# Kernel optimization log

Hardware: AMD Instinct MI355X
Metric: run time of the kernel (lower is better)

Reference implementation:

```python
import jax, jax.numpy as jnp
import numpy as np

B, S, H = 32, 2048, 1024


def setup_inputs() -> dict:
    key = jax.random.key(0)
    k1, k2, k3, k4, k5, k6 = jax.random.split(key, 6)
    hidden = jax.random.normal(k1, (B, H), dtype=jnp.float32)
    encoder_outputs = jax.random.normal(k2, (B, S, H), dtype=jnp.float32)
    lengths = jax.random.randint(k3, (B,), 1, S + 1, dtype=jnp.int64)
    scale = 1.0 / np.sqrt(H)
    Wq = jax.random.normal(k4, (H, H), dtype=jnp.float32) * scale
    Wk = jax.random.normal(k5, (H, H), dtype=jnp.float32) * scale
    v = jax.random.uniform(k6, (H,), dtype=jnp.float32)  # torch.rand init
    return {"hidden": hidden, "encoder_outputs": encoder_outputs,
            "lengths": lengths, "Wq": Wq, "Wk": Wk, "v": v}


def reference(hidden, encoder_outputs, lengths, Wq, Wk, v):
    # query: (B, 1, H); nn.Linear(bias=False) applies x @ W.T
    query = (hidden @ Wq.T)[:, None, :]
    keys = jnp.einsum('bsh,kh->bsk', encoder_outputs, Wk)  # (B, S, H)
    energy = jnp.tanh(query + keys)                         # (B, S, H)
    attn = jnp.einsum('bsh,h->bs', energy, v)               # (B, S)
    seq = encoder_outputs.shape[1]
    mask = jnp.arange(seq)[None, :] < lengths[:, None]      # (B, S)
    attn = jnp.where(mask, attn, -jnp.inf)
    return jax.nn.softmax(attn, axis=1)
```

## Files before the change

kernel.cpp:

```cpp
#include <hip/hip_runtime.h>
#include <hip/hip_fp16.h>
#include <stdint.h>

#define B_SZ 32
#define S_SZ 2048
#define H_SZ 1024
#define M_SZ (B_SZ * S_SZ)

typedef _Float16 half8 __attribute__((ext_vector_type(8)));
typedef float floatx4 __attribute__((ext_vector_type(4)));

struct h4 { _Float16 x, y, z, w; };

__global__ __launch_bounds__(256) void convert_f32_to_f16(
    const float* __restrict__ in, h4* __restrict__ out, int n4) {
  int i = blockIdx.x * blockDim.x + threadIdx.x;
  int stride = gridDim.x * blockDim.x;
  const float4* in4 = (const float4*)in;
  for (; i < n4; i += stride) {
    float4 f = in4[i];
    h4 o;
    o.x = (_Float16)f.x; o.y = (_Float16)f.y;
    o.z = (_Float16)f.z; o.w = (_Float16)f.w;
    out[i] = o;
  }
}

__global__ __launch_bounds__(256) void query_kernel(
    const float* __restrict__ hidden, const float* __restrict__ Wq,
    float* __restrict__ q) {
  int t = blockIdx.x * blockDim.x + threadIdx.x;
  int b = t & 31;
  int n = t >> 5;
  const float4* h4p = (const float4*)(hidden + (size_t)b * H_SZ);
  const float4* w4p = (const float4*)(Wq + (size_t)n * H_SZ);
  float acc = 0.f;
  #pragma unroll 4
  for (int i = 0; i < H_SZ / 4; ++i) {
    float4 h = h4p[i], w = w4p[i];
    acc = fmaf(h.x, w.x, acc);
    acc = fmaf(h.y, w.y, acc);
    acc = fmaf(h.z, w.z, acc);
    acc = fmaf(h.w, w.w, acc);
  }
  q[(size_t)b * H_SZ + n] = acc;
}

__device__ __forceinline__ void gl_lds16(const void* g, void* l) {
  __builtin_amdgcn_global_load_lds(
      (const __attribute__((address_space(1))) void*)g,
      (__attribute__((address_space(3))) void*)l,
      16, 0, 0);
}

__device__ __forceinline__ float fast_tanh(float x) {
  float ax = fabsf(x);
  float e = __expf(ax * -2.0f);
  float t = (1.0f - e) / (1.0f + e);
  return copysignf(t, x);
}

#define TILE 128
#define BK 32

__global__ __launch_bounds__(256) void fused_keys_kernel(
    const float* __restrict__ A,
    const _Float16* __restrict__ Bt,
    const float* __restrict__ q,
    const float* __restrict__ v,
    float* __restrict__ partial)
{
  __shared__ __align__(16) float    As[TILE * BK];
  __shared__ __align__(16) _Float16 Bs[TILE * BK];
  __shared__ float rowsum[TILE];
  __shared__ float q_l[TILE];
  __shared__ float v_l[TILE];

  const int tid  = threadIdx.x;
  const int w    = tid >> 6;
  const int lane = tid & 63;

  const int hw   = blockIdx.x;
  const int xcd  = hw & 7;
  const int slot = hw >> 3;
  const int bn   = slot & 7;
  const int bm   = ((slot >> 3) << 3) | xcd;

  const int R0   = bm * TILE;
  const int C0   = bn * TILE;
  const int bidx = R0 >> 11;

  if (tid < TILE) {
    q_l[tid] = q[(size_t)bidx * H_SZ + C0 + tid];
    v_l[tid] = v[C0 + tid];
    rowsum[tid] = 0.f;
  }

  const int wm = w >> 1, wn = w & 1;
  const int cL = lane & 15, quad = lane >> 4;

  floatx4 acc[4][4];
  #pragma unroll
  for (int m = 0; m < 4; ++m)
    #pragma unroll
    for (int n = 0; n < 4; ++n)
      acc[m][n] = (floatx4){0.f, 0.f, 0.f, 0.f};

  const int arow_l = lane >> 3;
  const int ap     = lane & 7;
  const int brow_l = lane >> 2;
  const int bp     = lane & 3;

  const float*    Ablk = A  + (size_t)R0 * H_SZ;
  const _Float16* Bblk = Bt + (size_t)C0 * H_SZ;

  for (int kt = 0; kt < H_SZ / BK; ++kt) {
    __syncthreads();
    const int kof = kt * BK;
    #pragma unroll
    for (int j = 0; j < 4; ++j) {
      const int row = w * 32 + j * 8 + arow_l;
      const int cg  = ap ^ ((row >> 1) & 7);
      gl_lds16(Ablk + (size_t)row * H_SZ + kof + cg * 4,
               (char*)As + (w * 256 + j * 64) * 16);
    }
    #pragma unroll
    for (int j = 0; j < 2; ++j) {
      const int row = w * 32 + j * 16 + brow_l;
      const int cg  = bp ^ ((row >> 1) & 3);
      gl_lds16(Bblk + (size_t)row * H_SZ + kof + cg * 8,
               (char*)Bs + (w * 128 + j * 64) * 16);
    }
    __syncthreads();

    half8 af[4], bf[4];
    #pragma unroll
    for (int m = 0; m < 4; ++m) {
      const int r = wm * 64 + m * 16 + cL;
      const int s = (r >> 1) & 7;
      const float4* Af = (const float4*)As + r * 8;
      float4 f0 = Af[(2 * quad) ^ s];
      float4 f1 = Af[(2 * quad + 1) ^ s];
      af[m] = (half8){(_Float16)f0.x, (_Float16)f0.y, (_Float16)f0.z, (_Float16)f0.w,
                      (_Float16)f1.x, (_Float16)f1.y, (_Float16)f1.z, (_Float16)f1.w};
    }
    #pragma unroll
    for (int n = 0; n < 4; ++n) {
      const int r = wn * 64 + n * 16 + cL;
      const int s = (r >> 1) & 3;
      bf[n] = *(const half8*)(Bs + r * 32 + ((quad ^ s) << 3));
    }
    #pragma unroll
    for (int m = 0; m < 4; ++m)
      #pragma unroll
      for (int n = 0; n < 4; ++n)
        acc[m][n] = __builtin_amdgcn_mfma_f32_16x16x32_f16(af[m], bf[n], acc[m][n], 0, 0, 0);
  }

  float qv[4], vv[4];
  #pragma unroll
  for (int n = 0; n < 4; ++n) {
    const int col = wn * 64 + n * 16 + cL;
    qv[n] = q_l[col];
    vv[n] = v_l[col];
  }
  #pragma unroll
  for (int m = 0; m < 4; ++m) {
    #pragma unroll
    for (int r = 0; r < 4; ++r) {
      float s = 0.f;
      #pragma unroll
      for (int n = 0; n < 4; ++n)
        s += vv[n] * fast_tanh(qv[n] + acc[m][n][r]);
      s += __shfl_xor(s, 1);
      s += __shfl_xor(s, 2);
      s += __shfl_xor(s, 4);
      s += __shfl_xor(s, 8);
      if (cL == 0)
        atomicAdd(&rowsum[wm * 64 + m * 16 + quad * 4 + r], s);
    }
  }
  __syncthreads();
  if (tid < TILE)
    partial[(size_t)bn * M_SZ + R0 + tid] = rowsum[tid];
}

__global__ __launch_bounds__(256) void softmax_kernel(
    const float* __restrict__ partial, const int* __restrict__ lengths,
    float* __restrict__ out) {
  __shared__ float wred[4];
  __shared__ float wsum[4];
  const int b = blockIdx.x;
  const int tid = threadIdx.x;
  const int len = lengths[b];

  float lg[8];
  #pragma unroll
  for (int i = 0; i < 8; ++i) {
    const int s = tid + i * 256;
    const size_t row = (size_t)b * S_SZ + s;
    float l = 0.f;
    #pragma unroll
    for (int nt = 0; nt < 8; ++nt) l += partial[(size_t)nt * M_SZ + row];
    lg[i] = (s < len) ? l : -INFINITY;
  }

  float mx = lg[0];
  #pragma unroll
  for (int i = 1; i < 8; ++i) mx = fmaxf(mx, lg[i]);
  #pragma unroll
  for (int off = 32; off; off >>= 1) mx = fmaxf(mx, __shfl_xor(mx, off));
  if ((tid & 63) == 0) wred[tid >> 6] = mx;
  __syncthreads();
  mx = fmaxf(fmaxf(wred[0], wred[1]), fmaxf(wred[2], wred[3]));

  float pe[8];
  float sum = 0.f;
  #pragma unroll
  for (int i = 0; i < 8; ++i) {
    float e = (lg[i] == -INFINITY) ? 0.f : __expf(lg[i] - mx);
    pe[i] = e;
    sum += e;
  }
  #pragma unroll
  for (int off = 32; off; off >>= 1) sum += __shfl_xor(sum, off);
  if ((tid & 63) == 0) wsum[tid >> 6] = sum;
  __syncthreads();
  sum = wsum[0] + wsum[1] + wsum[2] + wsum[3];
  const float inv = 1.0f / sum;

  #pragma unroll
  for (int i = 0; i < 8; ++i) {
    const int s = tid + i * 256;
    out[(size_t)b * S_SZ + s] = pe[i] * inv;
  }
}

extern "C" void kernel_launch(void* const* d_in, const int* in_sizes, int n_in,
                              void* d_out, int out_size, void* d_ws, size_t ws_size,
                              hipStream_t stream) {
  const float* hidden  = (const float*)d_in[0];
  const float* enc     = (const float*)d_in[1];
  const int*   lengths = (const int*)d_in[2];
  const float* Wq      = (const float*)d_in[3];
  const float* Wk      = (const float*)d_in[4];
  const float* v       = (const float*)d_in[5];
  float* out = (float*)d_out;

  char* ws = (char*)d_ws;
  _Float16* B16     = (_Float16*)ws;
  float*    q       = (float*)(ws + 2097152);
  float*    partial = (float*)(ws + 2097152 + 131072);

  convert_f32_to_f16<<<1024, 256, 0, stream>>>(Wk, (h4*)B16, (H_SZ * H_SZ) / 4);
  query_kernel<<<128, 256, 0, stream>>>(hidden, Wq, q);
  fused_keys_kernel<<<(M_SZ / TILE) * (H_SZ / TILE), 256, 0, stream>>>(enc, B16, q, v, partial);
  softmax_kernel<<<B_SZ, 256, 0, stream>>>(partial, lengths, out);
}
```

Measured before the change: 621.6 us.

## Double-buffer LDS tiles and remap warps to full-width row strips

Adds two LDS buffers for the A and B tiles so the async global-to-LDS load of the next K-slice is issued before computing the current one, dropping one barrier per iteration. It also reassigns each wave to a 32x128 strip (2x8 MFMA tiles) instead of a 64x64 quadrant, so every row's reduction over columns stays inside one wave. That lets the shared-memory rowsum and its atomics be removed and partial sums written straight to global. The cost is twice the LDS footprint, which may lower occupancy, and each wave now reads the whole B tile from LDS.

```diff
diff --git a/kernel.cpp b/kernel.cpp
--- a/kernel.cpp
+++ b/kernel.cpp
@@ -70,9 +70,8 @@
     const float* __restrict__ v,
     float* __restrict__ partial)
 {
-  __shared__ __align__(16) float    As[TILE * BK];
-  __shared__ __align__(16) _Float16 Bs[TILE * BK];
-  __shared__ float rowsum[TILE];
+  __shared__ __align__(16) float    As[2][TILE * BK];
+  __shared__ __align__(16) _Float16 Bs[2][TILE * BK];
   __shared__ float q_l[TILE];
   __shared__ float v_l[TILE];
 
@@ -93,17 +92,17 @@
   if (tid < TILE) {
     q_l[tid] = q[(size_t)bidx * H_SZ + C0 + tid];
     v_l[tid] = v[C0 + tid];
-    rowsum[tid] = 0.f;
-  }
-
-  const int wm = w >> 1, wn = w & 1;
-  const int cL = lane & 15, quad = lane >> 4;
-
-  floatx4 acc[4][4];
-  #pragma unroll
-  for (int m = 0; m < 4; ++m)
-    #pragma unroll
-    for (int n = 0; n < 4; ++n)
+  }
+
+  const int cL   = lane & 15, quad = lane >> 4;
+  const int sA   = cL >> 1;
+  const int sB   = sA & 3;
+
+  floatx4 acc[2][8];
+  #pragma unroll
+  for (int m = 0; m < 2; ++m)
+    #pragma unroll
+    for (int n = 0; n < 8; ++n)
       acc[m][n] = (floatx4){0.f, 0.f, 0.f, 0.f};
 
   const int arow_l = lane >> 3;
@@ -114,75 +113,81 @@
   const float*    Ablk = A  + (size_t)R0 * H_SZ;
   const _Float16* Bblk = Bt + (size_t)C0 * H_SZ;
 
-  for (int kt = 0; kt < H_SZ / BK; ++kt) {
-    __syncthreads();
-    const int kof = kt * BK;
+  auto stage = [&](int kt2, int b) {
+    const int kof = kt2 * BK;
     #pragma unroll
     for (int j = 0; j < 4; ++j) {
       const int row = w * 32 + j * 8 + arow_l;
       const int cg  = ap ^ ((row >> 1) & 7);
       gl_lds16(Ablk + (size_t)row * H_SZ + kof + cg * 4,
-               (char*)As + (w * 256 + j * 64) * 16);
+               (char*)&As[b][0] + (w * 256 + j * 64) * 16);
     }
     #pragma unroll
     for (int j = 0; j < 2; ++j) {
       const int row = w * 32 + j * 16 + brow_l;
       const int cg  = bp ^ ((row >> 1) & 3);
       gl_lds16(Bblk + (size_t)row * H_SZ + kof + cg * 8,
-               (char*)Bs + (w * 128 + j * 64) * 16);
-    }
-    __syncthreads();
-
-    half8 af[4], bf[4];
-    #pragma unroll
-    for (int m = 0; m < 4; ++m) {
-      const int r = wm * 64 + m * 16 + cL;
-      const int s = (r >> 1) & 7;
-      const float4* Af = (const float4*)As + r * 8;
-      float4 f0 = Af[(2 * quad) ^ s];
-      float4 f1 = Af[(2 * quad + 1) ^ s];
+               (char*)&Bs[b][0] + (w * 128 + j * 64) * 16);
+    }
+  };
+
+  auto compute = [&](int b) {
+    half8 af[2], bf[8];
+    #pragma unroll
+    for (int m = 0; m < 2; ++m) {
+      const int r = w * 32 + m * 16 + cL;
+      const float4* Af = (const float4*)&As[b][0] + r * 8;
+      float4 f0 = Af[(2 * quad) ^ sA];
+      float4 f1 = Af[(2 * quad + 1) ^ sA];
       af[m] = (half8){(_Float16)f0.x, (_Float16)f0.y, (_Float16)f0.z, (_Float16)f0.w,
                       (_Float16)f1.x, (_Float16)f1.y, (_Float16)f1.z, (_Float16)f1.w};
     }
     #pragma unroll
-    for (int n = 0; n < 4; ++n) {
-      const int r = wn * 64 + n * 16 + cL;
-      const int s = (r >> 1) & 3;
-      bf[n] = *(const half8*)(Bs + r * 32 + ((quad ^ s) << 3));
-    }
-    #pragma unroll
-    for (int m = 0; m < 4; ++m)
+    for (int n = 0; n < 8; ++n) {
+      const int r = n * 16 + cL;
+      bf[n] = *(const half8*)(&Bs[b][0] + r * 32 + ((quad ^ sB) << 3));
+    }
+    #pragma unroll
+    for (int m = 0; m < 2; ++m)
       #pragma unroll
-      for (int n = 0; n < 4; ++n)
+      for (int n = 0; n < 8; ++n)
         acc[m][n] = __builtin_amdgcn_mfma_f32_16x16x32_f16(af[m], bf[n], acc[m][n], 0, 0, 0);
-  }
-
-  float qv[4], vv[4];
-  #pragma unroll
-  for (int n = 0; n < 4; ++n) {
-    const int col = wn * 64 + n * 16 + cL;
+  };
+
+  stage(0, 0);
+  __syncthreads();
+  int cur = 0;
+  for (int kt = 0; kt < H_SZ / BK - 1; ++kt) {
+    stage(kt + 1, cur ^ 1);
+    compute(cur);
+    __syncthreads();
+    cur ^= 1;
+  }
+  compute(cur);
+
+  float qv[8], vv[8];
+  #pragma unroll
+  for (int n = 0; n < 8; ++n) {
+    const int col = n * 16 + cL;
     qv[n] = q_l[col];
     vv[n] = v_l[col];
   }
   #pragma unroll
-  for (int m = 0; m < 4; ++m) {
+  for (int m = 0; m < 2; ++m) {
     #pragma unroll
     for (int r = 0; r < 4; ++r) {
       float s = 0.f;
       #pragma unroll
-      for (int n = 0; n < 4; ++n)
+      for (int n = 0; n < 8; ++n)
         s += vv[n] * fast_tanh(qv[n] + acc[m][n][r]);
       s += __shfl_xor(s, 1);
       s += __shfl_xor(s, 2);
       s += __shfl_xor(s, 4);
       s += __shfl_xor(s, 8);
       if (cL == 0)
-        atomicAdd(&rowsum[wm * 64 + m * 16 + quad * 4 + r], s);
-    }
-  }
-  __syncthreads();
-  if (tid < TILE)
-    partial[(size_t)bn * M_SZ + R0 + tid] = rowsum[tid];
+        partial[(size_t)bn * M_SZ + R0 + w * 32 + m * 16 + quad * 4 + r] = s;
+    }
+  }
 }
 
 __global__ __launch_bounds__(256) void softmax_kernel(
```

Result: no change. 620.6 us (-0.2%).
